# Kernel optimization log

Measured on AMD Instinct MI355X. Metric: run time of the kernel, lower is better.

Reference implementation:

```python
import jax, jax.numpy as jnp
import numpy as np

FACTOR = 2
EPS = 1e-5


def _layernorm_last(x, w, b):
    # LayerNorm over the last dim only (torch nn.LayerNorm(size) with int size)
    mu = jnp.mean(x, axis=-1, keepdims=True)
    var = jnp.var(x, axis=-1, keepdims=True)
    return (x - mu) * jax.lax.rsqrt(var + EPS) * w + b


def setup_inputs() -> dict:
    key = jax.random.key(0)
    ks = jax.random.split(key, 12)
    B, C, H, W = 8, 512, 128, 128
    C8 = C // 8
    S = (H // FACTOR)  # = 64, LayerNorm size
    x = jax.random.normal(ks[0], (B, C, H, W), jnp.float32)
    s = 1.0 / np.sqrt(C)
    wq = jax.random.normal(ks[1], (C8, C), jnp.float32) * s
    bq = jax.random.normal(ks[2], (C8,), jnp.float32) * 0.02
    wk = jax.random.normal(ks[3], (C8, C), jnp.float32) * s
    bk = jax.random.normal(ks[4], (C8,), jnp.float32) * 0.02
    wv = jax.random.normal(ks[5], (C, C), jnp.float32) * s
    bv = jax.random.normal(ks[6], (C,), jnp.float32) * 0.02
    gamma = jax.random.normal(ks[7], (1,), jnp.float32) * 0.1
    ln_in_w = 1.0 + 0.1 * jax.random.normal(ks[8], (S,), jnp.float32)
    ln_in_b = 0.1 * jax.random.normal(ks[9], (S,), jnp.float32)
    ln_out_w = 1.0 + 0.1 * jax.random.normal(ks[10], (S,), jnp.float32)
    ln_out_b = 0.1 * jax.random.normal(ks[11], (S,), jnp.float32)
    return {"x": x, "wq": wq, "bq": bq, "wk": wk, "bk": bk, "wv": wv, "bv": bv,
            "gamma": gamma, "ln_in_w": ln_in_w, "ln_in_b": ln_in_b,
            "ln_out_w": ln_out_w, "ln_out_b": ln_out_b}


def reference(x, wq, bq, wk, bk, wv, bv, gamma, ln_in_w, ln_in_b, ln_out_w, ln_out_b):
    B, C, H, W = x.shape
    f = FACTOR
    Hp, Wp = H // f, W // f
    N = Hp * Wp
    # AvgPool2d(factor)
    xp = x.reshape(B, C, Hp, f, Wp, f).mean(axis=(3, 5))
    # LayerNorm over last dim (width)
    xn = _layernorm_last(xp, ln_in_w, ln_in_b)
    # 1x1 conv projections (einsum over channels)
    q = jnp.einsum('oc,bchw->bohw', wq, xn) + bq[None, :, None, None]
    k = jnp.einsum('oc,bchw->bohw', wk, xn) + bk[None, :, None, None]
    v = jnp.einsum('oc,bchw->bohw', wv, xn) + bv[None, :, None, None]
    q = q.reshape(B, -1, N)  # (B, C/8, N)
    k = k.reshape(B, -1, N)
    v = v.reshape(B, C, N)
    # energy = Q^T K, no scale (as in source)
    energy = jnp.einsum('bcn,bcm->bnm', q, k)  # (B, N, N)
    att = jax.nn.softmax(energy, axis=-1)
    # out = V @ att^T : out[b,c,n] = sum_m v[b,c,m] * att[b,n,m]
    out = jnp.einsum('bcm,bnm->bcn', v, att).reshape(B, C, Hp, Wp)
    out = _layernorm_last(out, ln_out_w, ln_out_b)
    # F.interpolate(scale_factor=f) -> nearest upsample
    out = jnp.repeat(jnp.repeat(out, f, axis=2), f, axis=3)
    return gamma * out + x
```

## Files before the change

### kernel.cpp

```cpp
#include <hip/hip_runtime.h>
#include <hip/hip_bf16.h>
#include <stdint.h>

#define BB 8
#define CC 512
#define HH 128
#define WW 128
#define HP 64
#define NN 4096
#define C8 64
#define EPSF 1e-5f
#define LOG2E 1.4426950408889634f
#define SM_SHIFT 46.0f

typedef __attribute__((ext_vector_type(8))) short short8;
typedef __attribute__((ext_vector_type(4))) float f32x4;

__device__ __forceinline__ float bf2f(ushort u) {
    union { uint i; float f; } x; x.i = ((uint)u) << 16; return x.f;
}
__device__ __forceinline__ ushort f2bf(float f) {
    uint i = __float_as_uint(f);
    return (ushort)((i + 0x7FFFu + ((i >> 16) & 1u)) >> 16);
}
__device__ __forceinline__ uint cvt_pk_bf16(float lo, float hi) {
    uint r;
    asm("v_cvt_pk_bf16_f32 %0, %1, %2" : "=v"(r) : "v"(lo), "v"(hi));
    return r;
}

__global__ __launch_bounds__(256) void pool_ln_kernel(
    const float* __restrict__ x, const float* __restrict__ lw,
    const float* __restrict__ lb, ushort* __restrict__ xn)
{
    int wid = threadIdx.x >> 6, lane = threadIdx.x & 63;
    int row = blockIdx.x * 4 + wid;
    int h = row & 63;
    int bc = row >> 6;
    const float* r0 = x + ((size_t)bc * 128 + 2 * h) * 128;
    const float* r1 = r0 + 128;
    float2 a0 = ((const float2*)r0)[lane];
    float2 a1 = ((const float2*)r1)[lane];
    float p = 0.25f * (a0.x + a0.y + a1.x + a1.y);
    float s = p, sq = p * p;
    #pragma unroll
    for (int m = 1; m < 64; m <<= 1) {
        s  += __shfl_xor(s,  m, 64);
        sq += __shfl_xor(sq, m, 64);
    }
    float mu  = s * (1.f / 64.f);
    float var = sq * (1.f / 64.f) - mu * mu;
    float inv = rsqrtf(var + EPSF);
    float v = (p - mu) * inv * lw[lane] + lb[lane];
    xn[(size_t)bc * NN + h * 64 + lane] = f2bf(v);
}

__global__ __launch_bounds__(256) void qkv_kernel(
    const ushort* __restrict__ xn,
    const float* __restrict__ wq, const float* __restrict__ bq,
    const float* __restrict__ wk, const float* __restrict__ bk,
    const float* __restrict__ wv, const float* __restrict__ bv,
    ushort* __restrict__ qt, ushort* __restrict__ kt, ushort* __restrict__ vo)
{
    __shared__ __align__(16) ushort As[64][40];
    __shared__ __align__(16) ushort Bs[64][66];
    int b = blockIdx.z, mt = blockIdx.y;
    int n0 = blockIdx.x * 64;
    const float* W; const float* bias;
    if (mt == 0)      { W = wq;                               bias = bq; }
    else if (mt == 1) { W = wk;                               bias = bk; }
    else              { W = wv + (size_t)(mt - 2) * 64 * 512; bias = bv + (mt - 2) * 64; }
    float mult = (mt == 0) ? LOG2E : 1.0f;
    const ushort* xb = xn + (size_t)b * CC * NN;
    int t = threadIdx.x;
    int lane = t & 63, wid = t >> 6;
    int wm = wid >> 1, wn = wid & 1;
    f32x4 acc[2][2] = {};

    for (int kc = 0; kc < 512; kc += 32) {
        {
            int row = t >> 2, k8 = (t & 3) * 8;
            const float* wp_ = &W[row * 512 + kc + k8];
            float4 f0 = *(const float4*)wp_;
            float4 f1 = *(const float4*)(wp_ + 4);
            ushort tmp[8] = { f2bf(f0.x * mult), f2bf(f0.y * mult), f2bf(f0.z * mult), f2bf(f0.w * mult),
                              f2bf(f1.x * mult), f2bf(f1.y * mult), f2bf(f1.z * mult), f2bf(f1.w * mult) };
            *(uint4*)&As[row][k8] = *(const uint4*)tmp;
        }
        {
            int c = t >> 3, n8 = (t & 7) * 8;
            uint4 v = *(const uint4*)&xb[(size_t)(kc + c) * NN + n0 + n8];
            const ushort* pv = (const ushort*)&v;
            #pragma unroll
            for (int e = 0; e < 8; e++) Bs[n8 + e][c] = pv[e];
        }
        __syncthreads();
        short8 a[2];
        #pragma unroll
        for (int fm = 0; fm < 2; fm++)
            a[fm] = *(const short8*)&As[wm * 32 + fm * 16 + (lane & 15)][(lane >> 4) * 8];
        short8 bb[2];
        #pragma unroll
        for (int fn = 0; fn < 2; fn++) {
            int col = wn * 32 + fn * 16 + (lane & 15);
            union { short8 v; uint u[4]; } bu;
            int c0 = (lane >> 4) * 8;
            #pragma unroll
            for (int p = 0; p < 4; p++)
                bu.u[p] = *(const uint*)&Bs[col][c0 + 2 * p];
            bb[fn] = bu.v;
        }
        #pragma unroll
        for (int fm = 0; fm < 2; fm++)
            #pragma unroll
            for (int fn = 0; fn < 2; fn++)
                acc[fm][fn] = __builtin_amdgcn_mfma_f32_16x16x32_bf16(a[fm], bb[fn], acc[fm][fn], 0, 0, 0);
        __syncthreads();
    }
    if (mt <= 1) {
        ushort* ot = ((mt == 0) ? qt : kt) + (size_t)b * NN * 64;
        #pragma unroll
        for (int fm = 0; fm < 2; fm++) {
            #pragma unroll
            for (int fn = 0; fn < 2; fn++) {
                int col = n0 + wn * 32 + fn * 16 + (lane & 15);
                int c0  = wm * 32 + fm * 16 + (lane >> 4) * 4;
                ushort tmp[4];
                #pragma unroll
                for (int r = 0; r < 4; r++)
                    tmp[r] = f2bf(acc[fm][fn][r] + bias[c0 + r] * mult);
                *(uint2*)&ot[(size_t)col * 64 + c0] = *(const uint2*)tmp;
            }
        }
    } else {
        ushort* outp = vo + (size_t)b * CC * NN + (size_t)(mt - 2) * 64 * NN;
        #pragma unroll
        for (int fm = 0; fm < 2; fm++) {
            #pragma unroll
            for (int fn = 0; fn < 2; fn++) {
                int col = n0 + wn * 32 + fn * 16 + (lane & 15);
                #pragma unroll
                for (int r = 0; r < 4; r++) {
                    int orow = wm * 32 + fm * 16 + (lane >> 4) * 4 + r;
                    outp[(size_t)orow * NN + col] = f2bf(acc[fm][fn][r] + bias[orow]);
                }
            }
        }
    }
}

__global__ __launch_bounds__(512, 4) void attn_kernel(
    const ushort* __restrict__ qt, const ushort* __restrict__ ktg,
    const ushort* __restrict__ vg, const float* __restrict__ x,
    const float* __restrict__ gamma_p,
    const float* __restrict__ lnw_g, const float* __restrict__ lnb_g,
    float* __restrict__ out)
{
    __shared__ __align__(16) ushort ktl[2][4096];
    __shared__ __align__(16) ushort Ps[2][64][68];
    __shared__ float row_lA[64], row_lB[64];
    __shared__ float lnw[64], lnb[64];

    int bid = blockIdx.x;
    int b     = bid & 7;
    int chalf = (bid >> 3) & 1;
    int h     = bid >> 4;
    int t = threadIdx.x, wid = t >> 6, lane = t & 63;
    int l15 = lane & 15, hig = lane >> 4;
    int w3 = wid & 3;
    int mh = wid >> 2;
    const ushort* ktb = ktg + (size_t)b * NN * 64;
    const ushort* vb  = vg  + (size_t)b * CC * NN;

    if (t < 64) { lnw[t] = lnw_g[t]; lnb[t] = lnb_g[t]; }

    const ushort* qrow = qt + (size_t)b * NN * 64 + (size_t)(h * 64 + w3 * 16 + l15) * 64;
    short8 qf0 = *(const short8*)&qrow[hig * 8];
    short8 qf1 = *(const short8*)&qrow[32 + hig * 8];

    int sm = t >> 3, sc = t & 7;
    int oo = sm * 64 + ((sc ^ (sm & 7)) * 8);

    f32x4 acc[4][2] = {};
    float lsum = 0.f;
    int cbase = chalf * 256 + wid * 32;
    int nrow = w3 * 16 + l15;
    int mq4 = hig * 4;

    const ushort* vp0 = vb + (size_t)(cbase + l15) * NN + hig * 8;
    const ushort* vp1 = vp0 + (size_t)16 * NN;
    const ushort* ktstage = ktb + 4096 + t * 8;

    int m_lo = (mh * 2) * 16 + l15;
    int m_hi = m_lo + 16;
    int q0a = m_lo * 64 + ((hig ^ (m_lo & 7)) * 8);
    int q0b = m_lo * 64 + (((hig + 4) ^ (m_lo & 7)) * 8);
    int q1a = m_hi * 64 + ((hig ^ (m_hi & 7)) * 8);
    int q1b = m_hi * 64 + (((hig + 4) ^ (m_hi & 7)) * 8);

    *(uint4*)&ktl[0][oo] = *(const uint4*)(ktb + t * 8);
    __syncthreads();

    #pragma unroll 2
    for (int mt2 = 0; mt2 < 64; mt2++) {
        const int cur = mt2 & 1, nxt = cur ^ 1;

        uint4 sa = *(const uint4*)ktstage;
        ktstage += 4096;
        short8 vreg[4];
        vreg[0] = *(const short8*)(vp0);
        vreg[1] = *(const short8*)(vp1);
        vreg[2] = *(const short8*)(vp0 + 32);
        vreg[3] = *(const short8*)(vp1 + 32);
        vp0 += 64; vp1 += 64;
        __builtin_amdgcn_sched_barrier(0);

        f32x4 sfT[2];
        {
            short8 k0 = *(const short8*)&ktl[cur][q0a];
            short8 k1 = *(const short8*)&ktl[cur][q0b];
            f32x4 s = {};
            s = __builtin_amdgcn_mfma_f32_16x16x32_bf16(k0, qf0, s, 0, 0, 0);
            s = __builtin_amdgcn_mfma_f32_16x16x32_bf16(k1, qf1, s, 0, 0, 0);
            sfT[0] = s;
        }
        {
            short8 k0 = *(const short8*)&ktl[cur][q1a];
            short8 k1 = *(const short8*)&ktl[cur][q1b];
            f32x4 s = {};
            s = __builtin_amdgcn_mfma_f32_16x16x32_bf16(k0, qf0, s, 0, 0, 0);
            s = __builtin_amdgcn_mfma_f32_16x16x32_bf16(k1, qf1, s, 0, 0, 0);
            sfT[1] = s;
        }

        #pragma unroll
        for (int lf = 0; lf < 2; lf++) {
            float e0 = exp2f(sfT[lf][0] - SM_SHIFT);
            float e1 = exp2f(sfT[lf][1] - SM_SHIFT);
            float e2 = exp2f(sfT[lf][2] - SM_SHIFT);
            float e3 = exp2f(sfT[lf][3] - SM_SHIFT);
            lsum += (e0 + e1) + (e2 + e3);
            uint2 pk;
            pk.x = cvt_pk_bf16(e0, e1);
            pk.y = cvt_pk_bf16(e2, e3);
            *(uint2*)&Ps[cur][nrow][(mh * 2 + lf) * 16 + mq4] = pk;
        }

        *(uint4*)&ktl[nxt][oo] = sa;

        __syncthreads();

        #pragma unroll
        for (int ks = 0; ks < 2; ks++) {
            short8 pa[4];
            #pragma unroll
            for (int f = 0; f < 4; f++)
                pa[f] = *(const short8*)&Ps[cur][f * 16 + l15][ks * 32 + hig * 8];
            #pragma unroll
            for (int g = 0; g < 2; g++)
                #pragma unroll
                for (int f = 0; f < 4; f++)
                    acc[f][g] = __builtin_amdgcn_mfma_f32_16x16x32_bf16(pa[f], vreg[ks * 2 + g], acc[f][g], 0, 0, 0);
        }
    }

    lsum += __shfl_xor(lsum, 16, 64);
    lsum += __shfl_xor(lsum, 32, 64);
    if (lane < 16) {
        if (mh == 0) row_lA[w3 * 16 + lane] = lsum;
        else         row_lB[w3 * 16 + lane] = lsum;
    }
    __syncthreads();

    float g = gamma_p[0];
    const float* xb2 = x + (size_t)b * CC * HH * WW;
    float* ob = out + (size_t)b * CC * HH * WW;
    float rl[4][4], lwv[4][4], lbv[4][4];
    #pragma unroll
    for (int fm = 0; fm < 4; fm++)
        #pragma unroll
        for (int r = 0; r < 4; r++) {
            int n = fm * 16 + hig * 4 + r;
            rl[fm][r] = 1.f / (row_lA[n] + row_lB[n]);
            lwv[fm][r] = lnw[n]; lbv[fm][r] = lnb[n];
        }
    #pragma unroll
    for (int fc = 0; fc < 2; fc++) {
        int c = cbase + fc * 16 + l15;
        float vv[4][4];
        float vsum = 0.f, vsq = 0.f;
        #pragma unroll
        for (int fm = 0; fm < 4; fm++)
            #pragma unroll
            for (int r = 0; r < 4; r++) {
                float v = acc[fm][fc][r] * rl[fm][r];
                vv[fm][r] = v; vsum += v; vsq += v * v;
            }
        vsum += __shfl_xor(vsum, 16, 64); vsum += __shfl_xor(vsum, 32, 64);
        vsq  += __shfl_xor(vsq,  16, 64); vsq  += __shfl_xor(vsq,  32, 64);
        float mu  = vsum * (1.f / 64.f);
        float var = vsq * (1.f / 64.f) - mu * mu;
        float inv = rsqrtf(var + EPSF);
        const float* xrow = xb2 + (size_t)c * HH * WW + (2 * h) * WW;
        float*       orow = ob  + (size_t)c * HH * WW + (2 * h) * WW;
        #pragma unroll
        for (int fm = 0; fm < 4; fm++) {
            int nbase = fm * 16 + hig * 4;
            float nv[4];
            #pragma unroll
            for (int r = 0; r < 4; r++)
                nv[r] = g * ((vv[fm][r] - mu) * inv * lwv[fm][r] + lbv[fm][r]);
            #pragma unroll
            for (int dh = 0; dh < 2; dh++) {
                float4 xv0 = *(const float4*)&xrow[dh * WW + 2 * nbase];
                float4 xv1 = *(const float4*)&xrow[dh * WW + 2 * nbase + 4];
                float4 o0, o1;
                o0.x = nv[0] + xv0.x; o0.y = nv[0] + xv0.y;
                o0.z = nv[1] + xv0.z; o0.w = nv[1] + xv0.w;
                o1.x = nv[2] + xv1.x; o1.y = nv[2] + xv1.y;
                o1.z = nv[3] + xv1.z; o1.w = nv[3] + xv1.w;
                *(float4*)&orow[dh * WW + 2 * nbase]     = o0;
                *(float4*)&orow[dh * WW + 2 * nbase + 4] = o1;
            }
        }
    }
}

extern "C" void kernel_launch(void* const* d_in, const int* in_sizes, int n_in,
                              void* d_out, int out_size, void* d_ws, size_t ws_size,
                              hipStream_t stream)
{
    (void)in_sizes; (void)n_in; (void)out_size; (void)ws_size;
    const float* x    = (const float*)d_in[0];
    const float* wq   = (const float*)d_in[1];
    const float* bq   = (const float*)d_in[2];
    const float* wk   = (const float*)d_in[3];
    const float* bk   = (const float*)d_in[4];
    const float* wv   = (const float*)d_in[5];
    const float* bv   = (const float*)d_in[6];
    const float* gam  = (const float*)d_in[7];
    const float* lniw = (const float*)d_in[8];
    const float* lnib = (const float*)d_in[9];
    const float* lnow = (const float*)d_in[10];
    const float* lnob = (const float*)d_in[11];
    float* out = (float*)d_out;

    char* ws = (char*)d_ws;
    ushort* xn = (ushort*)(ws);
    ushort* qt = (ushort*)(ws + 33554432u);
    ushort* kt = (ushort*)(ws + 37748736u);
    ushort* v  = (ushort*)(ws + 41943040u);

    pool_ln_kernel<<<65536, 256, 0, stream>>>(x, lniw, lnib, xn);
    qkv_kernel<<<dim3(64, 10, 8), 256, 0, stream>>>(xn, wq, bq, wk, bk, wv, bv, qt, kt, v);
    attn_kernel<<<1024, 512, 0, stream>>>(qt, kt, v, x, gam, lnow, lnob, out);
}
```

Baseline: 469.3 us.

## Merge channel halves per block and stream K tiles via direct global-to-LDS loads

```diff
diff --git a/kernel.cpp b/kernel.cpp
--- a/kernel.cpp
+++ b/kernel.cpp
@@ -162,9 +162,8 @@
     __shared__ float lnw[64], lnb[64];
 
     int bid = blockIdx.x;
-    int b     = bid & 7;
-    int chalf = (bid >> 3) & 1;
-    int h     = bid >> 4;
+    int b = bid & 7;
+    int h = bid >> 3;
     int t = threadIdx.x, wid = t >> 6, lane = t & 63;
     int l15 = lane & 15, hig = lane >> 4;
     int w3 = wid & 3;
@@ -178,18 +177,19 @@
     short8 qf0 = *(const short8*)&qrow[hig * 8];
     short8 qf1 = *(const short8*)&qrow[32 + hig * 8];
 
-    int sm = t >> 3, sc = t & 7;
-    int oo = sm * 64 + ((sc ^ (sm & 7)) * 8);
-
-    f32x4 acc[4][2] = {};
+    int soff = (wid * 8 + (lane >> 3)) * 64 + (((lane & 7) ^ ((lane >> 3) & 7)) * 8);
+    const ushort* ktsrc = ktb + soff;
+
+    f32x4 acc[4][4] = {};
     float lsum = 0.f;
-    int cbase = chalf * 256 + wid * 32;
+    int cbase = wid * 64;
     int nrow = w3 * 16 + l15;
     int mq4 = hig * 4;
 
-    const ushort* vp0 = vb + (size_t)(cbase + l15) * NN + hig * 8;
-    const ushort* vp1 = vp0 + (size_t)16 * NN;
-    const ushort* ktstage = ktb + 4096 + t * 8;
+    const ushort* vp[4];
+    #pragma unroll
+    for (int g = 0; g < 4; g++)
+        vp[g] = vb + (size_t)(cbase + g * 16 + l15) * NN + hig * 8;
 
     int m_lo = (mh * 2) * 16 + l15;
     int m_hi = m_lo + 16;
@@ -198,21 +198,23 @@
     int q1a = m_hi * 64 + ((hig ^ (m_hi & 7)) * 8);
     int q1b = m_hi * 64 + (((hig + 4) ^ (m_hi & 7)) * 8);
 
-    *(uint4*)&ktl[0][oo] = *(const uint4*)(ktb + t * 8);
+    __builtin_amdgcn_global_load_lds(
+        (const __attribute__((address_space(1))) void*)(const void*)ktsrc,
+        (__attribute__((address_space(3))) void*)(void*)&ktl[0][wid * 512], 16, 0, 0);
+    ktsrc += 4096;
     __syncthreads();
 
     #pragma unroll 2
     for (int mt2 = 0; mt2 < 64; mt2++) {
         const int cur = mt2 & 1, nxt = cur ^ 1;
 
-        uint4 sa = *(const uint4*)ktstage;
-        ktstage += 4096;
-        short8 vreg[4];
-        vreg[0] = *(const short8*)(vp0);
-        vreg[1] = *(const short8*)(vp1);
-        vreg[2] = *(const short8*)(vp0 + 32);
-        vreg[3] = *(const short8*)(vp1 + 32);
-        vp0 += 64; vp1 += 64;
+        __builtin_amdgcn_global_load_lds(
+            (const __attribute__((address_space(1))) void*)(const void*)ktsrc,
+            (__attribute__((address_space(3))) void*)(void*)&ktl[nxt][wid * 512], 16, 0, 0);
+        ktsrc += 4096;
+        short8 vr0[4];
+        #pragma unroll
+        for (int g = 0; g < 4; g++) vr0[g] = *(const short8*)vp[g];
         __builtin_amdgcn_sched_barrier(0);
 
         f32x4 sfT[2];
@@ -246,22 +248,38 @@
             *(uint2*)&Ps[cur][nrow][(mh * 2 + lf) * 16 + mq4] = pk;
         }
 
-        *(uint4*)&ktl[nxt][oo] = sa;
-
-        __syncthreads();
-
-        #pragma unroll
-        for (int ks = 0; ks < 2; ks++) {
+        asm volatile("s_waitcnt vmcnt(4) lgkmcnt(0)" ::: "memory");
+        __builtin_amdgcn_s_barrier();
+        __builtin_amdgcn_sched_barrier(0);
+
+        short8 vr1[4];
+        #pragma unroll
+        for (int g = 0; g < 4; g++) vr1[g] = *(const short8*)(vp[g] + 32);
+        __builtin_amdgcn_sched_barrier(0);
+        {
             short8 pa[4];
             #pragma unroll
             for (int f = 0; f < 4; f++)
-                pa[f] = *(const short8*)&Ps[cur][f * 16 + l15][ks * 32 + hig * 8];
-            #pragma unroll
-            for (int g = 0; g < 2; g++)
+                pa[f] = *(const short8*)&Ps[cur][f * 16 + l15][hig * 8];
+            #pragma unroll
+            for (int g = 0; g < 4; g++)
                 #pragma unroll
                 for (int f = 0; f < 4; f++)
-                    acc[f][g] = __builtin_amdgcn_mfma_f32_16x16x32_bf16(pa[f], vreg[ks * 2 + g], acc[f][g], 0, 0, 0);
-        }
+                    acc[f][g] = __builtin_amdgcn_mfma_f32_16x16x32_bf16(pa[f], vr0[g], acc[f][g], 0, 0, 0);
+        }
+        {
+            short8 pa[4];
+            #pragma unroll
+            for (int f = 0; f < 4; f++)
+                pa[f] = *(const short8*)&Ps[cur][f * 16 + l15][32 + hig * 8];
+            #pragma unroll
+            for (int g = 0; g < 4; g++)
+                #pragma unroll
+                for (int f = 0; f < 4; f++)
+                    acc[f][g] = __builtin_amdgcn_mfma_f32_16x16x32_bf16(pa[f], vr1[g], acc[f][g], 0, 0, 0);
+        }
+        #pragma unroll
+        for (int g = 0; g < 4; g++) vp[g] += 64;
     }
 
     lsum += __shfl_xor(lsum, 16, 64);
@@ -285,7 +303,7 @@
             lwv[fm][r] = lnw[n]; lbv[fm][r] = lnb[n];
         }
     #pragma unroll
-    for (int fc = 0; fc < 2; fc++) {
+    for (int fc = 0; fc < 4; fc++) {
         int c = cbase + fc * 16 + l15;
         float vv[4][4];
         float vsum = 0.f, vsq = 0.f;
@@ -353,5 +371,5 @@
 
     pool_ln_kernel<<<65536, 256, 0, stream>>>(x, lniw, lnib, xn);
     qkv_kernel<<<dim3(64, 10, 8), 256, 0, stream>>>(xn, wq, bq, wk, bk, wv, bv, qt, kt, v);
-    attn_kernel<<<1024, 512, 0, stream>>>(qt, kt, v, x, gam, lnow, lnob, out);
-}
+    attn_kernel<<<512, 512, 0, stream>>>(qt, kt, v, x, gam, lnow, lnob, out);
+}
```

New measurement: 661.8 us. 1.41x slower.
